# Kernel tuning notes

Measured on AMD Instinct MI355X. Metric: run time of the kernel, lower is better.

The kernel has to match this reference:

```python
import jax, jax.numpy as jnp
import numpy as np

N, L, D = 1024, 2048, 128

def setup_inputs() -> dict:
    key = jax.random.key(0)
    k1, k2, k3, k4 = jax.random.split(key, 4)
    input_seq = jax.random.normal(k1, (N, L, D), dtype=jnp.float32)
    cross_input = jax.random.normal(k2, (N, D), dtype=jnp.float32)
    # Learned params: W.weight [d,d] init N(0, 0.01), v [d] = randn*0.01
    W = jax.random.normal(k3, (D, D), dtype=jnp.float32) * 0.01
    v = jax.random.normal(k4, (D,), dtype=jnp.float32) * 0.01
    return {"input_seq": input_seq, "cross_input": cross_input, "W": W, "v": v}

def reference(input_seq, cross_input, W, v):
    # torch Linear: X @ W.T ; keys k = X W^T -> [n, L, d]
    k = jnp.einsum('nld,ed->nle', input_seq, W)
    # scores: z (n,1,d) @ k^T -> [n, L]
    scores = jnp.einsum('nd,nld->nl', cross_input, k)
    attn = jax.nn.softmax(scores, axis=-1)           # [n, L]
    ctx = jnp.einsum('nl,nld->nd', attn, input_seq)  # [n, d]
    out = jnp.einsum('nd,d->n', ctx, v)              # [n]
    # original returns (out @ v) with out shape [n,1,d] -> [n,1]
    return out[:, None]
```

## Files before the change

### kernel.cpp

```cpp
#include <hip/hip_runtime.h>
#include <math.h>

#define N_ 1024
#define L_ 2048
#define D_ 128
#define THREADS 256
#define GROUPS (THREADS / 32)

__global__ __launch_bounds__(THREADS) void attw_fused(
    const float* __restrict__ X,
    const float* __restrict__ Z,
    const float* __restrict__ W,
    const float* __restrict__ V,
    float* __restrict__ out)
{
    __shared__ float s_q[D_];
    __shared__ float s_v[D_];
    __shared__ float red_m[GROUPS], red_se[GROUPS], red_st[GROUPS];

    const int n = blockIdx.x;
    const int t = threadIdx.x;

    if (t < D_) {
        float acc = 0.f;
        const float* z = Z + n * D_;
        #pragma unroll 8
        for (int e = 0; e < D_; ++e)
            acc += z[e] * W[e * D_ + t];
        s_q[t] = acc;
    } else {
        s_v[t - D_] = V[t - D_];
    }
    __syncthreads();

    const int g    = t >> 5;
    const int lane = t & 31;
    const float4 q4 = ((const float4*)s_q)[lane];
    const float4 v4 = ((const float4*)s_v)[lane];

    float m = -3.0e38f, se = 0.f, st = 0.f;

    const float4* Xrow = (const float4*)(X + (size_t)n * L_ * D_);

    #pragma unroll 4
    for (int l = g; l < L_; l += GROUPS) {
        const float4 x = Xrow[l * 32 + lane];
        float s  = x.x * q4.x + x.y * q4.y + x.z * q4.z + x.w * q4.w;
        float tv = x.x * v4.x + x.y * v4.y + x.z * v4.z + x.w * v4.w;
        #pragma unroll
        for (int mask = 16; mask > 0; mask >>= 1) {
            s  += __shfl_xor(s,  mask, 32);
            tv += __shfl_xor(tv, mask, 32);
        }
        const float mnew  = fmaxf(m, s);
        const float scale = __expf(m - mnew);
        const float e     = __expf(s - mnew);
        se = se * scale + e;
        st = st * scale + e * tv;
        m  = mnew;
    }

    if (lane == 0) { red_m[g] = m; red_se[g] = se; red_st[g] = st; }
    __syncthreads();

    if (t == 0) {
        float M = red_m[0], SE = red_se[0], ST = red_st[0];
        #pragma unroll
        for (int i = 1; i < GROUPS; ++i) {
            const float m2  = red_m[i];
            const float Mn  = fmaxf(M, m2);
            const float sc1 = __expf(M - Mn);
            const float sc2 = __expf(m2 - Mn);
            SE = SE * sc1 + red_se[i] * sc2;
            ST = ST * sc1 + red_st[i] * sc2;
            M  = Mn;
        }
        out[n] = ST / SE;
    }
}

extern "C" void kernel_launch(void* const* d_in, const int* in_sizes, int n_in,
                              void* d_out, int out_size, void* d_ws, size_t ws_size,
                              hipStream_t stream) {
    const float* X = (const float*)d_in[0];
    const float* Z = (const float*)d_in[1];
    const float* W = (const float*)d_in[2];
    const float* V = (const float*)d_in[3];
    float* out = (float*)d_out;

    attw_fused<<<N_, THREADS, 0, stream>>>(X, Z, W, V, out);
}
```

Baseline: 1.348 ms.

## Split sequence dimension across blocks with partial softmax reduction kernels

The single fused kernel becomes three: a q projection kernel, a partial kernel that runs each batch row as 8 sequence chunks with online softmax, and a final kernel that merges the per-chunk (max, sum, weighted sum) triples. This raises the block count eightfold so more memory requests are in flight while streaming X. The cost is two extra kernel launches and workspace traffic for Q and the partials.

```diff
diff --git a/kernel.cpp b/kernel.cpp
--- a/kernel.cpp
+++ b/kernel.cpp
@@ -6,44 +6,45 @@
 #define D_ 128
 #define THREADS 256
 #define GROUPS (THREADS / 32)
+#define CHUNKS 8
+#define CHUNK_ROWS (L_ / CHUNKS)
 
-__global__ __launch_bounds__(THREADS) void attw_fused(
+__global__ __launch_bounds__(D_) void attw_q(
+    const float* __restrict__ Z, const float* __restrict__ W,
+    float* __restrict__ Q)
+{
+    const int n = blockIdx.x;
+    const int d = threadIdx.x;
+    const float* z = Z + n * D_;
+    float acc = 0.f;
+    #pragma unroll 8
+    for (int e = 0; e < D_; ++e)
+        acc += z[e] * W[e * D_ + d];
+    Q[n * D_ + d] = acc;
+}
+
+__global__ __launch_bounds__(THREADS) void attw_partial(
     const float* __restrict__ X,
-    const float* __restrict__ Z,
-    const float* __restrict__ W,
+    const float* __restrict__ Q,
     const float* __restrict__ V,
-    float* __restrict__ out)
+    float4* __restrict__ P)
 {
-    __shared__ float s_q[D_];
-    __shared__ float s_v[D_];
-    __shared__ float red_m[GROUPS], red_se[GROUPS], red_st[GROUPS];
-
-    const int n = blockIdx.x;
+    const int c = blockIdx.x;
+    const int n = blockIdx.y;
     const int t = threadIdx.x;
-
-    if (t < D_) {
-        float acc = 0.f;
-        const float* z = Z + n * D_;
-        #pragma unroll 8
-        for (int e = 0; e < D_; ++e)
-            acc += z[e] * W[e * D_ + t];
-        s_q[t] = acc;
-    } else {
-        s_v[t - D_] = V[t - D_];
-    }
-    __syncthreads();
-
     const int g    = t >> 5;
     const int lane = t & 31;
-    const float4 q4 = ((const float4*)s_q)[lane];
-    const float4 v4 = ((const float4*)s_v)[lane];
+
+    const float4 q4 = ((const float4*)(Q + n * D_))[lane];
+    const float4 v4 = ((const float4*)V)[lane];
 
     float m = -3.0e38f, se = 0.f, st = 0.f;
 
     const float4* Xrow = (const float4*)(X + (size_t)n * L_ * D_);
+    const int l0 = c * CHUNK_ROWS;
 
     #pragma unroll 4
-    for (int l = g; l < L_; l += GROUPS) {
+    for (int l = l0 + g; l < l0 + CHUNK_ROWS; l += GROUPS) {
         const float4 x = Xrow[l * 32 + lane];
         float s  = x.x * q4.x + x.y * q4.y + x.z * q4.z + x.w * q4.w;
         float tv = x.x * v4.x + x.y * v4.y + x.z * v4.z + x.w * v4.w;
@@ -60,6 +61,7 @@
         m  = mnew;
     }
 
+    __shared__ float red_m[GROUPS], red_se[GROUPS], red_st[GROUPS];
     if (lane == 0) { red_m[g] = m; red_se[g] = se; red_st[g] = st; }
     __syncthreads();
 
@@ -69,14 +71,35 @@
         for (int i = 1; i < GROUPS; ++i) {
             const float m2  = red_m[i];
             const float Mn  = fmaxf(M, m2);
-            const float sc1 = __expf(M - Mn);
-            const float sc2 = __expf(m2 - Mn);
-            SE = SE * sc1 + red_se[i] * sc2;
-            ST = ST * sc1 + red_st[i] * sc2;
+            const float s1  = __expf(M - Mn);
+            const float s2  = __expf(m2 - Mn);
+            SE = SE * s1 + red_se[i] * s2;
+            ST = ST * s1 + red_st[i] * s2;
             M  = Mn;
         }
-        out[n] = ST / SE;
+        P[n * CHUNKS + c] = make_float4(M, SE, ST, 0.f);
     }
+}
+
+__global__ __launch_bounds__(256) void attw_final(
+    const float4* __restrict__ P, float* __restrict__ out)
+{
+    const int n = blockIdx.x * blockDim.x + threadIdx.x;
+    if (n >= N_) return;
+    const float4* p = P + n * CHUNKS;
+    float4 a = p[0];
+    float M = a.x, SE = a.y, ST = a.z;
+    #pragma unroll
+    for (int i = 1; i < CHUNKS; ++i) {
+        const float4 b = p[i];
+        const float Mn = fmaxf(M, b.x);
+        const float s1 = __expf(M - Mn);
+        const float s2 = __expf(b.x - Mn);
+        SE = SE * s1 + b.y * s2;
+        ST = ST * s1 + b.z * s2;
+        M  = Mn;
+    }
+    out[n] = ST / SE;
 }
 
 extern "C" void kernel_launch(void* const* d_in, const int* in_sizes, int n_in,
@@ -88,5 +111,10 @@
     const float* V = (const float*)d_in[3];
     float* out = (float*)d_out;
 
-    attw_fused<<<N_, THREADS, 0, stream>>>(X, Z, W, V, out);
+    float*  Q = (float*)d_ws;
+    float4* P = (float4*)((char*)d_ws + (size_t)N_ * D_ * sizeof(float));
+
+    attw_q<<<N_, D_, 0, stream>>>(Z, W, Q);
+    attw_partial<<<dim3(CHUNKS, N_), THREADS, 0, stream>>>(X, Q, V, P);
+    attw_final<<<(N_ + 255) / 256, 256, 0, stream>>>(P, out);
 }
```

Measured after the change: 1.328 ms. About the same (-1.5%).
